# Kernel optimization log

Hardware: AMD Instinct MI355X
Metric: run time of the kernel (lower is better)

The kernel has to match this reference:

```python
import jax, jax.numpy as jnp
import numpy as np

D = 2048
H = 16
HD = 128
INNER = H * HD
EPS = 1e-6


def rmsnorm(x, w):
    var = jnp.mean(x * x, axis=-1, keepdims=True)
    return x * jax.lax.rsqrt(var + EPS) * w


def setup_inputs() -> dict:
    key = jax.random.key(0)
    ks = jax.random.split(key, 10)
    B, T, N_ws, T_corr = 2, 2048, 64, 512
    scale = 1.0 / np.sqrt(D)
    return {
        "hidden_states": jax.random.normal(ks[0], (B, T, D), jnp.float32),
        "workspace": jax.random.normal(ks[1], (B, N_ws, D), jnp.float32),
        "correction_tokens": jax.random.normal(ks[2], (B, T_corr, D), jnp.float32),
        "correction_mask": jax.random.randint(ks[3], (B, T_corr), 0, 2, jnp.int32),
        "ln_q_w": jnp.ones((D,), jnp.float32),
        "ln_kv_w": jnp.ones((D,), jnp.float32),
        "Wq": jax.random.normal(ks[4], (D, INNER), jnp.float32) * scale,
        "Wk": jax.random.normal(ks[5], (D, INNER), jnp.float32) * scale,
        "Wv": jax.random.normal(ks[6], (D, INNER), jnp.float32) * scale,
        "Wo": jax.random.normal(ks[7], (INNER, D), jnp.float32) * scale,
    }


def reference(hidden_states, workspace, correction_tokens, correction_mask,
              ln_q_w, ln_kv_w, Wq, Wk, Wv, Wo):
    B, T, _ = hidden_states.shape
    N_ws = workspace.shape[1]
    # kv context = [workspace ; correction_tokens]
    kv_context = jnp.concatenate([workspace, correction_tokens], axis=1)  # (B, N_kv, D)
    N_kv = kv_context.shape[1]
    ws_mask = jnp.ones((B, N_ws), hidden_states.dtype)
    kv_mask = jnp.concatenate([ws_mask, correction_mask.astype(hidden_states.dtype)], axis=1)  # (B, N_kv)

    h = rmsnorm(hidden_states, ln_q_w)
    kv = rmsnorm(kv_context, ln_kv_w)

    q = (h @ Wq).reshape(B, T, H, HD)        # (B,T,H,hd)
    k = (kv @ Wk).reshape(B, N_kv, H, HD)
    v = (kv @ Wv).reshape(B, N_kv, H, HD)

    scores = jnp.einsum("bthd,bshd->bhts", q, k) / np.sqrt(HD)  # (B,H,T,N_kv)
    mask = (kv_mask != 0)[:, None, None, :]                      # (B,1,1,N_kv)
    scores = jnp.where(mask, scores, -jnp.inf)
    attn = jax.nn.softmax(scores, axis=-1)
    attn = jnp.nan_to_num(attn, nan=0.0)
    # dropout is identity in eval mode
    out = jnp.einsum("bhts,bshd->bthd", attn, v).reshape(B, T, INNER)
    return out @ Wo
```

## Files before the change

kernel.cpp:

```cpp
#include <hip/hip_runtime.h>
#include <hip/hip_bf16.h>
#include <math.h>

typedef __bf16 bf16;
typedef __attribute__((ext_vector_type(8))) __bf16 bf16x8;
typedef __attribute__((ext_vector_type(4))) __bf16 bf16x4;
typedef __attribute__((ext_vector_type(4))) float f32x4;

#define D_DIM 2048
#define NKV   576

__device__ inline void gld_lds16(const void* g, void* l) {
    void* gg = const_cast<void*>(g);
    __builtin_amdgcn_global_load_lds(
        (__attribute__((address_space(1))) void*)gg,
        (__attribute__((address_space(3))) void*)l, 16, 0, 0);
}

#define PH_BARRIER() do { __builtin_amdgcn_s_barrier(); asm volatile("" ::: "memory"); } while (0)
#define VMCNT(n)     asm volatile("s_waitcnt vmcnt(" #n ")" ::: "memory")

__global__ __launch_bounds__(256) void prep(
    const float* __restrict__ hidden, const float* __restrict__ wsp,
    const float* __restrict__ corr, const float* __restrict__ lnq,
    const float* __restrict__ lnkv,
    const float* __restrict__ Wq, const float* __restrict__ Wk,
    const float* __restrict__ Wv, const float* __restrict__ Wo,
    bf16* __restrict__ hb, bf16* __restrict__ kvb,
    bf16* __restrict__ WqT, bf16* __restrict__ WkvT, bf16* __restrict__ WoT)
{
    __shared__ float tl[64][65];
    __shared__ float p[4];
    const int id = blockIdx.x, t = threadIdx.x;

    if (id < 4096) {
        const int wz = id >> 10, idx = id & 1023;
        const int wy = idx >> 5, wx = idx & 31;
        const float* in; bf16* out;
        switch (wz) {
            case 0:  in = Wq; out = WqT; break;
            case 1:  in = Wk; out = WkvT; break;
            case 2:  in = Wv; out = WkvT + 2048ull * 2048; break;
            default: in = Wo; out = WoT; break;
        }
        const int r0 = wy * 64, c0 = wx * 64;
        const int tr = t >> 4, tc = (t & 15) * 4;
#pragma unroll
        for (int q = 0; q < 4; ++q) {
            const int r = tr + q * 16;
            float4 v = *(const float4*)(in + (long)(r0 + r) * 2048 + c0 + tc);
            tl[r][tc] = v.x; tl[r][tc + 1] = v.y;
            tl[r][tc + 2] = v.z; tl[r][tc + 3] = v.w;
        }
        __syncthreads();
#pragma unroll
        for (int q = 0; q < 2; ++q) {
            const int rc = (t >> 3) + q * 32;
            const int c8 = (t & 7) * 8;
            bf16x8 o;
#pragma unroll
            for (int i = 0; i < 8; ++i) o[i] = (bf16)tl[c8 + i][rc];
            *(bf16x8*)(out + (long)(c0 + rc) * 2048 + r0 + c8) = o;
        }
        return;
    }

    const int rr0 = id - 4096;
    const float* xr; const float* w; bf16* yr;
    if (rr0 < 4096) {
        xr = hidden + (long)rr0 * D_DIM; w = lnq; yr = hb + (long)rr0 * D_DIM;
    } else if (rr0 < 4224) {
        const int rr = rr0 - 4096;
        xr = wsp + (long)rr * D_DIM; w = lnkv;
        yr = kvb + ((long)(rr >> 6) * NKV + (rr & 63)) * D_DIM;
    } else {
        const int rr = rr0 - 4224;
        xr = corr + (long)rr * D_DIM; w = lnkv;
        yr = kvb + ((long)(rr >> 9) * NKV + 64 + (rr & 511)) * D_DIM;
    }

    float4 v0 = *(const float4*)(xr + t * 4);
    float4 v1 = *(const float4*)(xr + 1024 + t * 4);
    float ss = v0.x * v0.x + v0.y * v0.y + v0.z * v0.z + v0.w * v0.w
             + v1.x * v1.x + v1.y * v1.y + v1.z * v1.z + v1.w * v1.w;
#pragma unroll
    for (int off = 32; off; off >>= 1) ss += __shfl_xor(ss, off);
    if ((t & 63) == 0) p[t >> 6] = ss;
    __syncthreads();
    const float rs = rsqrtf((p[0] + p[1] + p[2] + p[3]) * (1.0f / 2048.0f) + 1e-6f);

    float4 w0 = *(const float4*)(w + t * 4);
    float4 w1 = *(const float4*)(w + 1024 + t * 4);
    bf16x4 o0 = { (bf16)(v0.x * rs * w0.x), (bf16)(v0.y * rs * w0.y),
                  (bf16)(v0.z * rs * w0.z), (bf16)(v0.w * rs * w0.w) };
    bf16x4 o1 = { (bf16)(v1.x * rs * w1.x), (bf16)(v1.y * rs * w1.y),
                  (bf16)(v1.z * rs * w1.z), (bf16)(v1.w * rs * w1.w) };
    *(bf16x4*)(yr + t * 4) = o0;
    *(bf16x4*)(yr + 1024 + t * 4) = o1;
}

__global__ __launch_bounds__(512, 2) void proj_all(
    const bf16* __restrict__ hb, const bf16* __restrict__ kvb,
    const bf16* __restrict__ WqT, const bf16* __restrict__ WkvT,
    bf16* __restrict__ qb, bf16* __restrict__ kb, bf16* __restrict__ vtb)
{
    __shared__ __align__(16) bf16 smem[4][16384];
    bf16* const EA = smem[0]; bf16* const EB = smem[1];
    bf16* const OA = smem[2]; bf16* const OB = smem[3];

    const int id0 = blockIdx.x;
    const int id = (id0 & 7) * 26 + (id0 >> 3);
    const bf16 *A, *B; int m0, n0; bool isQ;
    if (id < 128) {
        isQ = true;  A = hb;  B = WqT;
        m0 = (id >> 3) * 256; n0 = (id & 7) * 256;
    } else {
        const int kd = id - 128;
        isQ = false; A = kvb; B = WkvT;
        m0 = (kd >> 4) * 256; n0 = (kd & 15) * 256;
    }

    const int tid = threadIdx.x, lane = tid & 63, w = tid >> 6;
    const int wm = (w >> 2) * 128, wn = (w & 3) * 64;
    const int fr = lane & 15, fg = lane >> 4;

    f32x4 acc[8][4] = {};
    bf16x8 af[4][2], bg[4][2];

    const int aoff0 = (wm + fr) * 64 + (fg ^ (fr & 7)) * 8;
    const int boff0 = (wn + fr) * 64 + (fg ^ (fr & 7)) * 8;
    const int aoff1 = aoff0 ^ 32, boff1 = boff0 ^ 32;
    const bf16* const pAE[2] = { EA + aoff0, EA + aoff1 };
    const bf16* const pAO[2] = { OA + aoff0, OA + aoff1 };
    const bf16* const pBE[2] = { EB + boff0, EB + boff1 };
    const bf16* const pBO[2] = { OB + boff0, OB + boff1 };

    const long toff = (long)(tid >> 3) * 2048 + (((tid & 7) ^ ((tid >> 3) & 7)) * 8);
    const bf16* const gA0 = A + (long)m0 * 2048 + toff;
    const bf16* const gA1 = gA0 + 262144;
    const bf16* const gB0 = B + (long)n0 * 2048 + toff;
    const bf16* const gB1 = gB0 + 262144;
    bf16* const dT = (bf16*)smem + tid * 8;

    auto stage2 = [&](const bf16* g, int k, int dslot) {
        gld_lds16(g + k, dT + dslot);
        gld_lds16(g + 131072 + k, dT + dslot + 4096);
    };
    enum { sEA0 = 0, sEA1 = 8192, sEB0 = 16384, sEB1 = 24576,
           sOA0 = 32768, sOA1 = 40960, sOB0 = 49152, sOB1 = 57344 };

    auto load_af = [&](const bf16* const p[2], int ib) {
#pragma unroll
        for (int i = 0; i < 4; ++i)
#pragma unroll
            for (int s = 0; s < 2; ++s)
                af[i][s] = *(const bf16x8*)(p[s] + (ib + i) * 1024);
    };
    auto load_bg4 = [&](const bf16* const p[2]) {
#pragma unroll
        for (int j = 0; j < 4; ++j)
#pragma unroll
            for (int s = 0; s < 2; ++s)
                bg[j][s] = *(const bf16x8*)(p[s] + j * 1024);
    };
    auto mfma16 = [&](int ib, int jb) {
        __builtin_amdgcn_s_setprio(1);
#pragma unroll
        for (int s = 0; s < 2; ++s)
#pragma unroll
            for (int i = 0; i < 4; ++i)
#pragma unroll
                for (int j = 0; j < 2; ++j)
                    acc[ib + i][jb + j] = __builtin_amdgcn_mfma_f32_16x16x32_bf16(
                        af[i][s], bg[jb + j][s], acc[ib + i][jb + j], 0, 0, 0);
        __builtin_amdgcn_s_setprio(0);
    };

    stage2(gA0, 0, sEA0); stage2(gA1, 0, sEA1);
    stage2(gB0, 0, sEB0); stage2(gB1, 0, sEB1);
    stage2(gB0, 64, sOB0); stage2(gB1, 64, sOB1);
    stage2(gA0, 64, sOA0);
    VMCNT(6);
    PH_BARRIER();

    for (int it = 0; it < 15; ++it) {
        const int kO = it * 128 + 64, kE2 = it * 128 + 128, kO2 = it * 128 + 192;
        load_af(pAE, 0); load_bg4(pBE);
        stage2(gA1, kO, sOA1);
        PH_BARRIER(); mfma16(0, 0); PH_BARRIER();
        stage2(gB0, kE2, sEB0);
        PH_BARRIER(); mfma16(0, 2); PH_BARRIER();
        load_af(pAE, 4);
        stage2(gB1, kE2, sEB1);
        PH_BARRIER(); mfma16(4, 2); PH_BARRIER();
        stage2(gA0, kE2, sEA0);
        PH_BARRIER(); mfma16(4, 0); VMCNT(6); PH_BARRIER();
        load_af(pAO, 0); load_bg4(pBO);
        stage2(gA1, kE2, sEA1);
        PH_BARRIER(); mfma16(0, 0); PH_BARRIER();
        stage2(gB0, kO2, sOB0);
        PH_BARRIER(); mfma16(0, 2); PH_BARRIER();
        load_af(pAO, 4);
        stage2(gB1, kO2, sOB1);
        PH_BARRIER(); mfma16(4, 2); PH_BARRIER();
        stage2(gA0, kO2, sOA0);
        PH_BARRIER(); mfma16(4, 0); VMCNT(6); PH_BARRIER();
    }
    {
        load_af(pAE, 0); load_bg4(pBE);
        stage2(gA1, 1984, sOA1);
        PH_BARRIER(); mfma16(0, 0); PH_BARRIER();
        PH_BARRIER(); mfma16(0, 2); PH_BARRIER();
        load_af(pAE, 4);
        PH_BARRIER(); mfma16(4, 2); PH_BARRIER();
        PH_BARRIER(); mfma16(4, 0); VMCNT(0); PH_BARRIER();
        load_af(pAO, 0); load_bg4(pBO);
        PH_BARRIER(); mfma16(0, 0); PH_BARRIER();
        PH_BARRIER(); mfma16(0, 2); PH_BARRIER();
        load_af(pAO, 4);
        PH_BARRIER(); mfma16(4, 2); PH_BARRIER();
        PH_BARRIER(); mfma16(4, 0); PH_BARRIER();
    }

    __syncthreads();

    const int er = fg * 4;
    if (isQ || n0 < 2048) {
        bf16* C = isQ ? qb : kb;
        const int mlim = isQ ? 4096 : 1152;
#pragma unroll
        for (int i = 0; i < 8; ++i)
#pragma unroll
            for (int j = 0; j < 4; ++j) {
                const int n = n0 + wn + j * 16 + fr;
#pragma unroll
                for (int r = 0; r < 4; ++r) {
                    const int m = m0 + wm + i * 16 + er + r;
                    if (m < mlim)
                        C[(long)m * 2048 + n] = (bf16)acc[i][j][r];
                }
            }
        return;
    }

    bf16* T = &smem[0][0];
#pragma unroll
    for (int p2 = 0; p2 < 2; ++p2) {
        if (p2) __syncthreads();
        if ((wn >> 7) == p2) {
            const int nb = wn - p2 * 128;
#pragma unroll
            for (int i = 0; i < 8; ++i)
#pragma unroll
                for (int j = 0; j < 4; ++j) {
                    const int nl = nb + j * 16 + fr;
#pragma unroll
                    for (int r = 0; r < 4; ++r)
                        T[nl * 264 + wm + i * 16 + er + r] = (bf16)acc[i][j][r];
                }
        }
        __syncthreads();
        const int hh = (n0 - 2048 + p2 * 128) >> 7;
        for (int e = tid; e < 128 * 64; e += 512) {
            const int d = e >> 6, mg = (e & 63) * 4;
            const int mm = m0 + mg;
            if (mm < 1152) {
                bf16x4 val = *(const bf16x4*)(T + d * 264 + mg);
                const int bb = mm >= NKV;
                const int s = mm - bb * NKV;
                *(bf16x4*)(vtb + ((long)((bb * 16 + hh) * 128 + d)) * NKV + s) = val;
            }
        }
    }
}

__global__ __launch_bounds__(512, 2) void gemm_final(
    const bf16* __restrict__ Ag, const bf16* __restrict__ Bg, float* __restrict__ C)
{
    __shared__ __align__(16) bf16 smem[49152];
    bf16* const EA = smem;           bf16* const EB = smem + 16384;
    bf16* const OA = smem + 24576;   bf16* const OB = smem + 40960;

    const int id0 = blockIdx.x;
    const int id = (id0 & 7) * 32 + (id0 >> 3);
    const int m0 = (id >> 4) * 256, n0 = (id & 15) * 128;

    const int tid = threadIdx.x, lane = tid & 63, w = tid >> 6;
    const int wm = (w >> 1) * 64, wn = (w & 1) * 64;
    const int fr = lane & 15, fg = lane >> 4;

    f32x4 acc[4][4] = {};
    bf16x8 af[2][2], bg[4][2];

    const int aoff0 = (wm + fr) * 64 + (fg ^ (fr & 7)) * 8;
    const int boff0 = (wn + fr) * 64 + (fg ^ (fr & 7)) * 8;
    const int aoff1 = aoff0 ^ 32, boff1 = boff0 ^ 32;
    const bf16* const pAE[2] = { EA + aoff0, EA + aoff1 };
    const bf16* const pAO[2] = { OA + aoff0, OA + aoff1 };
    const bf16* const pBE[2] = { EB + boff0, EB + boff1 };
    const bf16* const pBO[2] = { OB + boff0, OB + boff1 };

    const long toff = (long)(tid >> 3) * 2048 + (((tid & 7) ^ ((tid >> 3) & 7)) * 8);
    const bf16* const gA0 = Ag + (long)m0 * 2048 + toff;
    const bf16* const gA1 = gA0 + 262144;
    const bf16* const gB0 = Bg + (long)n0 * 2048 + toff;
    bf16* const dT = smem + tid * 8;

    auto stage2 = [&](const bf16* g, int k, int dslot) {
        gld_lds16(g + k, dT + dslot);
        gld_lds16(g + 131072 + k, dT + dslot + 4096);
    };
    enum { sEA0 = 0, sEA1 = 8192, sEB0 = 16384,
           sOA0 = 24576, sOA1 = 32768, sOB0 = 40960 };

    auto load_af = [&](const bf16* const p[2], int ib) {
#pragma unroll
        for (int i = 0; i < 2; ++i)
#pragma unroll
            for (int s = 0; s < 2; ++s)
                af[i][s] = *(const bf16x8*)(p[s] + (ib + i) * 1024);
    };
    auto load_bg4 = [&](const bf16* const p[2]) {
#pragma unroll
        for (int j = 0; j < 4; ++j)
#pragma unroll
            for (int s = 0; s < 2; ++s)
                bg[j][s] = *(const bf16x8*)(p[s] + j * 1024);
    };
    auto mfma8 = [&](int ib, int jb) {
        __builtin_amdgcn_s_setprio(1);
#pragma unroll
        for (int s = 0; s < 2; ++s)
#pragma unroll
            for (int i = 0; i < 2; ++i)
#pragma unroll
                for (int j = 0; j < 2; ++j)
                    acc[ib + i][jb + j] = __builtin_amdgcn_mfma_f32_16x16x32_bf16(
                        af[i][s], bg[jb + j][s], acc[ib + i][jb + j], 0, 0, 0);
        __builtin_amdgcn_s_setprio(0);
    };

    stage2(gA0, 0, sEA0); stage2(gA1, 0, sEA1);
    stage2(gB0, 0, sEB0);
    stage2(gB0, 64, sOB0); stage2(gA0, 64, sOA0);
    VMCNT(4);
    PH_BARRIER();

    for (int it = 0; it < 15; ++it) {
        const int kO = it * 128 + 64, kE2 = it * 128 + 128, kO2 = it * 128 + 192;
        load_af(pAE, 0); load_bg4(pBE);
        stage2(gA1, kO, sOA1);
        PH_BARRIER(); mfma8(0, 0); PH_BARRIER();
        stage2(gB0, kE2, sEB0);
        PH_BARRIER(); mfma8(0, 2); PH_BARRIER();
        load_af(pAE, 2);
        PH_BARRIER(); mfma8(2, 2); PH_BARRIER();
        stage2(gA0, kE2, sEA0);
        PH_BARRIER(); mfma8(2, 0); VMCNT(4); PH_BARRIER();
        load_af(pAO, 0); load_bg4(pBO);
        stage2(gA1, kE2, sEA1);
        PH_BARRIER(); mfma8(0, 0); PH_BARRIER();
        stage2(gB0, kO2, sOB0);
        PH_BARRIER(); mfma8(0, 2); PH_BARRIER();
        load_af(pAO, 2);
        PH_BARRIER(); mfma8(2, 2); PH_BARRIER();
        stage2(gA0, kO2, sOA0);
        PH_BARRIER(); mfma8(2, 0); VMCNT(4); PH_BARRIER();
    }
    {
        load_af(pAE, 0); load_bg4(pBE);
        stage2(gA1, 1984, sOA1);
        PH_BARRIER(); mfma8(0, 0); PH_BARRIER();
        PH_BARRIER(); mfma8(0, 2); PH_BARRIER();
        load_af(pAE, 2);
        PH_BARRIER(); mfma8(2, 2); PH_BARRIER();
        PH_BARRIER(); mfma8(2, 0); VMCNT(0); PH_BARRIER();
        load_af(pAO, 0); load_bg4(pBO);
        PH_BARRIER(); mfma8(0, 0); PH_BARRIER();
        PH_BARRIER(); mfma8(0, 2); PH_BARRIER();
        load_af(pAO, 2);
        PH_BARRIER(); mfma8(2, 2); PH_BARRIER();
        PH_BARRIER(); mfma8(2, 0); PH_BARRIER();
    }

    __syncthreads();

    const int er = fg * 4;
#pragma unroll
    for (int i = 0; i < 4; ++i)
#pragma unroll
        for (int j = 0; j < 4; ++j) {
            const int n = n0 + wn + j * 16 + fr;
#pragma unroll
            for (int r = 0; r < 4; ++r)
                C[(long)(m0 + wm + i * 16 + er + r) * 2048 + n] = acc[i][j][r];
        }
}

__global__ __launch_bounds__(512, 4) void flash_attn(
    const bf16* __restrict__ Q, const bf16* __restrict__ K,
    const bf16* __restrict__ VT, const int* __restrict__ cmask,
    bf16* __restrict__ O)
{
    __shared__ __align__(16) bf16 Ks[64 * 128];
    __shared__ __align__(16) bf16 VTs[128 * 64];
    __shared__ __align__(16) bf16 Ps[128 * 72];

    const int qt = blockIdx.x, h = blockIdx.y, b = blockIdx.z;
    const int tid = threadIdx.x, lane = tid & 63, w = tid >> 6;
    const int fr = lane & 15, fg = lane >> 4;

    const bf16* qbase = Q + ((long)(b * 2048 + qt * 128)) * 2048 + h * 128;
    bf16x8 qf[4];
#pragma unroll
    for (int s = 0; s < 4; ++s)
        qf[s] = *(const bf16x8*)(qbase + (long)(w * 16 + fr) * 2048 + s * 32 + fg * 8);

    float m_r[4], l_r[4];
    f32x4 acc_o[8];
#pragma unroll
    for (int r = 0; r < 4; ++r) { m_r[r] = -3.0e38f; l_r[r] = 0.f; }
#pragma unroll
    for (int j = 0; j < 8; ++j) acc_o[j] = (f32x4){0.f, 0.f, 0.f, 0.f};

    const float scale2 = 0.12752792330124195f;
    const bf16* kbase = K + (long)b * NKV * 2048 + h * 128;
    const bf16* vbase = VT + ((long)(b * 16 + h)) * 128 * NKV;
    const int* const cm = cmask + b * 512;

    for (int kc = 0; kc < 9; ++kc) {
        const int kv0 = kc * 64;
#pragma unroll
        for (int p = 0; p < 2; ++p) {
            const int c = p * 512 + tid;
            const int r = c >> 4, cs = c & 15, cl = cs ^ (r & 15);
            gld_lds16(kbase + (long)(kv0 + r) * 2048 + cl * 8, Ks + c * 8);
        }
#pragma unroll
        for (int p = 0; p < 2; ++p) {
            const int c = p * 512 + tid;
            const int r = c >> 3, cs = c & 7, cl = cs ^ (r & 7);
            gld_lds16(vbase + (long)r * NKV + kv0 + cl * 8, VTs + c * 8);
        }
        __syncthreads();

        f32x4 acc_s[4] = {};
#pragma unroll
        for (int s = 0; s < 4; ++s) {
#pragma unroll
            for (int j = 0; j < 4; ++j) {
                bf16x8 bgv = *(const bf16x8*)(Ks +
                    ((j * 16 + fr) * 16 + ((s * 4 + fg) ^ fr)) * 8);
                acc_s[j] = __builtin_amdgcn_mfma_f32_16x16x32_bf16(qf[s], bgv, acc_s[j], 0, 0, 0);
            }
        }

        float bias[4];
#pragma unroll
        for (int j = 0; j < 4; ++j) {
            const int kv = kv0 + j * 16 + fr;
            const bool valid = (kv < 64) || (cm[kv - 64] != 0);
            bias[j] = valid ? 0.f : -1e30f;
        }
        float s_f[4][4];
        float mc[4] = {-3.0e38f, -3.0e38f, -3.0e38f, -3.0e38f};
#pragma unroll
        for (int j = 0; j < 4; ++j)
#pragma unroll
            for (int r = 0; r < 4; ++r) {
                float v = fmaf(acc_s[j][r], scale2, bias[j]);
                s_f[j][r] = v; mc[r] = fmaxf(mc[r], v);
            }
#pragma unroll
        for (int r = 0; r < 4; ++r) {
            mc[r] = fmaxf(mc[r], __shfl_xor(mc[r], 1));
            mc[r] = fmaxf(mc[r], __shfl_xor(mc[r], 2));
            mc[r] = fmaxf(mc[r], __shfl_xor(mc[r], 4));
            mc[r] = fmaxf(mc[r], __shfl_xor(mc[r], 8));
        }
        float alpha[4];
#pragma unroll
        for (int r = 0; r < 4; ++r) {
            const float mn = fmaxf(m_r[r], mc[r]);
            alpha[r] = __builtin_amdgcn_exp2f(m_r[r] - mn);
            m_r[r] = mn;
        }
        float rs[4] = {0.f, 0.f, 0.f, 0.f};
#pragma unroll
        for (int j = 0; j < 4; ++j)
#pragma unroll
            for (int r = 0; r < 4; ++r) {
                const float pv = __builtin_amdgcn_exp2f(s_f[j][r] - m_r[r]);
                s_f[j][r] = pv; rs[r] += pv;
            }
#pragma unroll
        for (int r = 0; r < 4; ++r) {
            rs[r] += __shfl_xor(rs[r], 1);
            rs[r] += __shfl_xor(rs[r], 2);
            rs[r] += __shfl_xor(rs[r], 4);
            rs[r] += __shfl_xor(rs[r], 8);
            l_r[r] = l_r[r] * alpha[r] + rs[r];
        }
#pragma unroll
        for (int j = 0; j < 8; ++j)
#pragma unroll
            for (int r = 0; r < 4; ++r) acc_o[j][r] *= alpha[r];

#pragma unroll
        for (int j = 0; j < 4; ++j)
#pragma unroll
            for (int r = 0; r < 4; ++r)
                Ps[(w * 16 + fg * 4 + r) * 72 + j * 16 + fr] = (bf16)s_f[j][r];

#pragma unroll
        for (int s2 = 0; s2 < 2; ++s2) {
            bf16x8 afv = *(const bf16x8*)(Ps + (w * 16 + fr) * 72 + s2 * 32 + fg * 8);
#pragma unroll
            for (int jd = 0; jd < 8; ++jd) {
                bf16x8 bgv = *(const bf16x8*)(VTs +
                    ((jd * 16 + fr) * 8 + ((s2 * 4 + fg) ^ (fr & 7))) * 8);
                acc_o[jd] = __builtin_amdgcn_mfma_f32_16x16x32_bf16(afv, bgv, acc_o[jd], 0, 0, 0);
            }
        }
        __syncthreads();
    }

    bf16* obase = O + ((long)(b * 2048 + qt * 128)) * 2048 + h * 128;
#pragma unroll
    for (int r = 0; r < 4; ++r) {
        const float inv = 1.0f / l_r[r];
        const int row = w * 16 + fg * 4 + r;
#pragma unroll
        for (int jd = 0; jd < 8; ++jd)
            obase[(long)row * 2048 + jd * 16 + fr] = (bf16)(acc_o[jd][r] * inv);
    }
}

extern "C" void kernel_launch(void* const* d_in, const int* in_sizes, int n_in,
                              void* d_out, int out_size, void* d_ws, size_t ws_size,
                              hipStream_t stream)
{
    const float* hidden = (const float*)d_in[0];
    const float* wsp    = (const float*)d_in[1];
    const float* corr   = (const float*)d_in[2];
    const int*   cmask  = (const int*)d_in[3];
    const float* lnq    = (const float*)d_in[4];
    const float* lnkv   = (const float*)d_in[5];
    const float* Wq     = (const float*)d_in[6];
    const float* Wk     = (const float*)d_in[7];
    const float* Wv     = (const float*)d_in[8];
    const float* Wo     = (const float*)d_in[9];
    float* out = (float*)d_out;

    char* ws = (char*)d_ws;
    size_t off = 0;
    auto alloc = [&](size_t sz) { void* p = ws + off; off += (sz + 255) & ~(size_t)255; return p; };

    bf16* WqT   = (bf16*)alloc(2048ull * 2048 * 2);
    bf16* WkvT  = (bf16*)alloc(4096ull * 2048 * 2);
    bf16* WoT   = (bf16*)alloc(2048ull * 2048 * 2);
    bf16* hb    = (bf16*)alloc(4096ull * 2048 * 2);
    bf16* kvb   = (bf16*)alloc(1280ull * 2048 * 2);
    bf16* qb    = (bf16*)alloc(4096ull * 2048 * 2);
    bf16* kb    = (bf16*)alloc(1152ull * 2048 * 2);
    bf16* vtb   = (bf16*)alloc(4096ull * NKV * 2);
    bf16* aob   = (bf16*)alloc(4096ull * 2048 * 2);

    prep<<<9344, 256, 0, stream>>>(hidden, wsp, corr, lnq, lnkv,
                                   Wq, Wk, Wv, Wo, hb, kvb, WqT, WkvT, WoT);
    proj_all<<<208, 512, 0, stream>>>(hb, kvb, WqT, WkvT, qb, kb, vtb);
    flash_attn<<<dim3(16, 16, 2), 512, 0, stream>>>(qb, kb, vtb, cmask, aob);
    gemm_final<<<256, 512, 0, stream>>>(aob, WoT, out);
}
```

Measured before the change: 289.9 us.

## Double-buffer K/V tiles in flash attention and swizzle P buffer

Flash attention now keeps two LDS buffers for K and V^T and issues direct global-to-LDS loads two tiles ahead. It uses vmcnt waits and raw barriers so the loads overlap with the MFMA and softmax work. The padded P staging buffer is replaced by an unpadded 64-wide buffer with an XOR swizzle to avoid bank conflicts. LDS use per block grows, which may limit occupancy under the 512x4 launch bounds.

```diff
diff --git a/kernel.cpp b/kernel.cpp
--- a/kernel.cpp
+++ b/kernel.cpp
@@ -402,9 +402,9 @@
     const bf16* __restrict__ VT, const int* __restrict__ cmask,
     bf16* __restrict__ O)
 {
-    __shared__ __align__(16) bf16 Ks[64 * 128];
-    __shared__ __align__(16) bf16 VTs[128 * 64];
-    __shared__ __align__(16) bf16 Ps[128 * 72];
+    __shared__ __align__(16) bf16 Ks[2][64 * 128];
+    __shared__ __align__(16) bf16 VTs[2][128 * 64];
+    __shared__ __align__(16) bf16 Ps[128 * 64];
 
     const int qt = blockIdx.x, h = blockIdx.y, b = blockIdx.z;
     const int tid = threadIdx.x, lane = tid & 63, w = tid >> 6;
@@ -428,28 +428,37 @@
     const bf16* vbase = VT + ((long)(b * 16 + h)) * 128 * NKV;
     const int* const cm = cmask + b * 512;
 
-    for (int kc = 0; kc < 9; ++kc) {
-        const int kv0 = kc * 64;
+    auto stageK = [&](int kv0, int bi) {
 #pragma unroll
         for (int p = 0; p < 2; ++p) {
             const int c = p * 512 + tid;
             const int r = c >> 4, cs = c & 15, cl = cs ^ (r & 15);
-            gld_lds16(kbase + (long)(kv0 + r) * 2048 + cl * 8, Ks + c * 8);
-        }
+            gld_lds16(kbase + (long)(kv0 + r) * 2048 + cl * 8, Ks[bi] + c * 8);
+        }
+    };
+    auto stageV = [&](int kv0, int bi) {
 #pragma unroll
         for (int p = 0; p < 2; ++p) {
             const int c = p * 512 + tid;
             const int r = c >> 3, cs = c & 7, cl = cs ^ (r & 7);
-            gld_lds16(vbase + (long)r * NKV + kv0 + cl * 8, VTs + c * 8);
-        }
-        __syncthreads();
+            gld_lds16(vbase + (long)r * NKV + kv0 + cl * 8, VTs[bi] + c * 8);
+        }
+    };
+
+    stageK(0, 0);  stageV(0, 0);
+    stageK(64, 1); stageV(64, 1);
+    VMCNT(4);
+    PH_BARRIER();
+
+    for (int kc = 0; kc < 9; ++kc) {
+        const int kv0 = kc * 64, cur = kc & 1;
 
         f32x4 acc_s[4] = {};
 #pragma unroll
         for (int s = 0; s < 4; ++s) {
 #pragma unroll
             for (int j = 0; j < 4; ++j) {
-                bf16x8 bgv = *(const bf16x8*)(Ks +
+                bf16x8 bgv = *(const bf16x8*)(Ks[cur] +
                     ((j * 16 + fr) * 16 + ((s * 4 + fg) ^ fr)) * 8);
                 acc_s[j] = __builtin_amdgcn_mfma_f32_16x16x32_bf16(qf[s], bgv, acc_s[j], 0, 0, 0);
             }
@@ -509,20 +518,33 @@
 #pragma unroll
         for (int j = 0; j < 4; ++j)
 #pragma unroll
-            for (int r = 0; r < 4; ++r)
-                Ps[(w * 16 + fg * 4 + r) * 72 + j * 16 + fr] = (bf16)s_f[j][r];
+            for (int r = 0; r < 4; ++r) {
+                const int row = w * 16 + fg * 4 + r;
+                Ps[row * 64 + ((j * 16 + fr) ^ ((row & 7) << 3))] = (bf16)s_f[j][r];
+            }
 
 #pragma unroll
         for (int s2 = 0; s2 < 2; ++s2) {
-            bf16x8 afv = *(const bf16x8*)(Ps + (w * 16 + fr) * 72 + s2 * 32 + fg * 8);
+            const int prow = w * 16 + fr;
+            bf16x8 afv = *(const bf16x8*)(Ps + prow * 64 +
+                ((s2 * 32 + fg * 8) ^ ((prow & 7) << 3)));
 #pragma unroll
             for (int jd = 0; jd < 8; ++jd) {
-                bf16x8 bgv = *(const bf16x8*)(VTs +
+                bf16x8 bgv = *(const bf16x8*)(VTs[cur] +
                     ((jd * 16 + fr) * 8 + ((s2 * 4 + fg) ^ (fr & 7))) * 8);
                 acc_o[jd] = __builtin_amdgcn_mfma_f32_16x16x32_bf16(afv, bgv, acc_o[jd], 0, 0, 0);
             }
         }
-        __syncthreads();
+
+        PH_BARRIER();
+        if (kc <= 6) {
+            stageK(kv0 + 128, cur);
+            stageV(kv0 + 128, cur);
+            VMCNT(4);
+        } else {
+            VMCNT(0);
+        }
+        PH_BARRIER();
     }
 
     bf16* obase = O + ((long)(b * 2048 + qt * 128)) * 2048 + h * 128;
```

Measured after the change: 299.6 us. +3.3%, slower.
